# Kernel optimization log

Hardware: AMD Instinct MI355X
Metric: run time of the kernel (lower is better)

The kernel has to match this reference:

```python
import jax, jax.numpy as jnp
import numpy as np

B, N = 32, 512


def _stick_breaking(b, x_mask):
    """Row-major stick-breaking recurrence, O(N^2) sequential steps.

    Equivalent to the TF while_loop: for step in range(N*N), m=step//N, n=step%N:
      fut      = max(0, x_mask[:,m,n+1:] - sum_{m'<m} x[:,m',n+1:])  (col partial sums)
      mfm      = sum_j fut_j
      row_sum  = sum_{n'<n} x[:,m,n']
      col_sum  = sum_{m'<m} x[:,m',n]
      lower    = mask[m,n]*max(0, 1 - row_sum - mfm)
      upper    = mask[m,n]*min(1 - row_sum, 1 - col_sum)
      x[m,n]   = lower + b[m,n]*(upper - lower)
    Key insight: during row m the column partial sums are constant, so the
    future-mass terms for every n can be precomputed as an exclusive reverse
    cumsum; only the within-row dependency (row_sum) needs a scan.
    """
    Bb, Nn, _ = b.shape
    dt = b.dtype

    def row_step(col_sums, inputs):
        b_row, mask_row = inputs                      # [B, N] each
        fut = jnp.maximum(0.0, mask_row - col_sums)   # [B, N]
        # mfm[:, n] = sum_{j > n} fut[:, j]  (exclusive reverse cumsum)
        mfm = jnp.flip(jnp.cumsum(jnp.flip(fut, -1), axis=-1), -1) - fut

        def col_step(row_sum, inp):
            b_mn, m_mn, mfm_n, cs_n = inp             # [B] each
            lower = m_mn * jnp.maximum(0.0, 1.0 - row_sum - mfm_n)
            upper = m_mn * jnp.minimum(1.0 - row_sum, 1.0 - cs_n)
            p = lower + b_mn * (upper - lower)
            return row_sum + p, p

        _, row = jax.lax.scan(
            col_step,
            jnp.zeros((Bb,), dt),
            (b_row.T, mask_row.T, mfm.T, col_sums.T),
        )
        row = row.T                                   # [B, N]
        return col_sums + row, row

    _, rows = jax.lax.scan(
        row_step,
        jnp.zeros((Bb, Nn), dt),
        (jnp.swapaxes(b, 0, 1), jnp.swapaxes(x_mask, 0, 1)),
    )
    return jnp.swapaxes(rows, 0, 1)                   # [B, N, N]


def setup_inputs() -> dict:
    key = jax.random.key(0)
    k1, _ = jax.random.split(key)
    x = jax.random.normal(k1, (B, N, N), dtype=jnp.float32)
    x_mask = jnp.ones((B, N, N), dtype=jnp.float32)
    return {"x": x, "x_mask": x_mask}


def reference(x, x_mask):
    # layer.call applies sigmoid to the logits before stick-breaking
    return _stick_breaking(jax.nn.sigmoid(x), x_mask)
```

## Files before the change

kernel.cpp:

```cpp
#include <hip/hip_runtime.h>
#include <type_traits>

#define NBATCH 32
#define NDIM 512
#define NFAST 448
#define NWAVE 8


template <int CTRL, int RMASK>
__device__ __forceinline__ float dpp_add(float x) {
  int t = __builtin_amdgcn_update_dpp(0, __float_as_int(x), CTRL, RMASK, 0xf,
                                      false);
  return x + __int_as_float(t);
}

__device__ __forceinline__ float prefix_inc(float x) {
  x = dpp_add<0x111, 0xf>(x);
  x = dpp_add<0x112, 0xf>(x);
  x = dpp_add<0x114, 0xf>(x);
  x = dpp_add<0x118, 0xf>(x);
  x = dpp_add<0x142, 0xa>(x);
  x = dpp_add<0x143, 0xc>(x);
  return x;
}

__device__ __forceinline__ float wave_shr1(float x, float fill) {
  return __int_as_float(__builtin_amdgcn_update_dpp(
      __float_as_int(fill), __float_as_int(x), 0x138 , 0xf, 0xf,
      false));
}

template <int CTRL, int RMASK>
__device__ __forceinline__ void aff_step(float& A, float& B) {
  float Ae = __int_as_float(__builtin_amdgcn_update_dpp(
      __float_as_int(1.0f), __float_as_int(A), CTRL, RMASK, 0xf, false));
  float Be = __int_as_float(__builtin_amdgcn_update_dpp(
      0, __float_as_int(B), CTRL, RMASK, 0xf, false));
  B = fmaf(A, Be, B);
  A = A * Ae;
}

__device__ __forceinline__ void wg_barrier() {
  asm volatile("s_waitcnt lgkmcnt(0)" ::: "memory");
  __builtin_amdgcn_s_barrier();
  asm volatile("" ::: "memory");
}

__global__ __launch_bounds__(512, 2)
void sb_kernel(const float* __restrict__ x, const float* __restrict__ xm,
               float* __restrict__ out) {
  const int tid = (int)threadIdx.x;
  const int lane = tid & 63;
  const int w = __builtin_amdgcn_readfirstlane(tid >> 6);
  const size_t base =
      (size_t)blockIdx.x * NDIM * NDIM + (size_t)(w * 64 + lane);
  const float* xb = x + base;
  const float* mb = xm + base;
  float* ob = out + base;

  __shared__ float4 recs[NFAST];
  __shared__ alignas(16) float ex_sa[NWAVE];
  __shared__ alignas(16) float ex_S[NWAVE];
  __shared__ alignas(16) float ex_A[NWAVE];
  __shared__ alignas(16) float ex_B[NWAVE];

  float w8, t8, sa;
  float fu = 0.0f, S = 0.0f;
  float c1, c2, oc2;

  float X0 = *(xb);
  float M0 = *(mb);
  float a1 = xb[NDIM], b1 = mb[NDIM];
  float a2 = xb[2 * NDIM], b2 = mb[2 * NDIM];
  float a3 = xb[3 * NDIM], b3 = mb[3 * NDIM];
  float sx0 = a1, sm0 = b1, sx1 = a1, sm1 = b1, sx2 = a1, sm2 = b1, sx3 = a1,
        sm3 = b1;
  switch (w & 3) {
    case 0:
      sx1 = a1; sm1 = b1; sx2 = a2; sm2 = b2; sx3 = a3; sm3 = b3;
      break;
    case 1:
      sx2 = a1; sm2 = b1; sx3 = a2; sm3 = b2; sx0 = a3; sm0 = b3;
      break;
    case 2:
      sx3 = a1; sm3 = b1; sx0 = a2; sm0 = b2; sx1 = a3; sm1 = b3;
      break;
    default:
      sx0 = a1; sm0 = b1; sx1 = a2; sm1 = b2; sx2 = a3; sm2 = b3;
      break;
  }

  {
    float sg = __builtin_amdgcn_rcpf(1.0f + __expf(-X0));
    c2 = M0 * sg;
    oc2 = 1.0f - c2;
    c1 = M0 - c2;
    w8 = 1.0f;
    t8 = c2;
    sa = t8;
  }

  auto fast_step = [&](int t, float& LX, float& LM, const float& CX,
                       const float& CM) {
    const int m = t - w;
    if ((unsigned)m < (unsigned)NFAST) {
      float4 r = make_float4(1.0f, 0.0f, 0.0f, 0.0f);
      if (w > 0) r = recs[m];
      const size_t nro = (size_t)(m + 4) * NDIM;
      LX = xb[nro];
      LM = mb[nro];

      float PA = prefix_inc(sa);

      float sg = __builtin_amdgcn_rcpf(1.0f + __expf(-CX));
      float c2n = CM * sg;
      float oc2n = 1.0f - c2n;
      float c1n = CM - c2n;

      float uin = fmaxf(1.0f - (r.z + (PA - sa)), 0.0f);

      bool pW = w8 < uin;
      float A = pW ? 1.0f : oc2;
      float Bv = pW ? (-t8) : 0.0f;

      aff_step<0x111, 0xf>(A, Bv);
      aff_step<0x112, 0xf>(A, Bv);
      aff_step<0x114, 0xf>(A, Bv);
      aff_step<0x118, 0xf>(A, Bv);
      aff_step<0x142, 0xa>(A, Bv);
      aff_step<0x143, 0xc>(A, Bv);
      float Aex = wave_shr1(A, 1.0f);
      float Bex = wave_shr1(Bv, 0.0f);

      if (w < NWAVE - 1 && lane == 63)
        recs[m] = make_float4(A * r.x, fmaf(A, r.y, Bv), r.z + PA, 0.0f);

      float E = r.x + r.y;
      float e = fminf(fmaxf(fmaf(Aex, E, Bex), 0.0f), 1.0f);

      float p = c2 * fminf(e, w8);
      w8 -= p;
      ob[(size_t)m * NDIM] = p;

      t8 = c2n * w8;
      sa = t8;
      c2 = c2n;
      oc2 = oc2n;
      c1 = c1n;
    }
    wg_barrier();
  };

#pragma unroll 1
  for (int t = 0; t < NFAST + NWAVE; t += 4) {
    fast_step(t + 0, sx0, sm0, sx1, sm1);
    fast_step(t + 1, sx1, sm1, sx2, sm2);
    fast_step(t + 2, sx2, sm2, sx3, sm3);
    fast_step(t + 3, sx3, sm3, sx0, sm0);
  }

  sx1 = xb[(size_t)449 * NDIM];
  sm1 = mb[(size_t)449 * NDIM];
  sx2 = xb[(size_t)450 * NDIM];
  sm2 = mb[(size_t)450 * NDIM];
  sx3 = xb[(size_t)451 * NDIM];
  sm3 = mb[(size_t)451 * NDIM];
  {
    float om = 1.0f - c1 - c2;
    fu = fmaxf(w8 - om, 0.0f);
    S = fu;
  }

  auto row_full = [&](int m, float& WX, float& WM, const float& RX,
                      const float& RM) {
    const size_t nro = (size_t)((m + 4) & (NDIM - 1)) * NDIM;
    WX = xb[nro];
    WM = mb[nro];

    float PS = prefix_inc(S);
    float PA = prefix_inc(sa);

    if (lane == 63) {
      ex_sa[w] = PA;
      ex_S[w] = PS;
    }
    wg_barrier();

    float4 sl = *(const float4*)&ex_sa[0];
    float4 sh = *(const float4*)&ex_sa[4];
    float4 Sl = *(const float4*)&ex_S[0];
    float4 Sh = *(const float4*)&ex_S[4];
    float off_sa = 0.0f, off_S = 0.0f;
    if (w > 0) { off_sa += sl.x; off_S += Sl.x; }
    if (w > 1) { off_sa += sl.y; off_S += Sl.y; }
    if (w > 2) { off_sa += sl.z; off_S += Sl.z; }
    if (w > 3) { off_sa += sl.w; off_S += Sl.w; }
    if (w > 4) { off_sa += sh.x; off_S += Sh.x; }
    if (w > 5) { off_sa += sh.y; off_S += Sh.y; }
    if (w > 6) { off_sa += sh.z; off_S += Sh.z; }
    float Tg = ((Sl.x + Sl.y) + (Sl.z + Sl.w)) + ((Sh.x + Sh.y) + (Sh.z + Sh.w));

    float uin = fmaxf(1.0f - (off_sa + (PA - sa)), 0.0f);
    float R_ = (Tg - off_S) - PS;
    float nc1m = -c1 * R_;

    bool pW = w8 < uin;
    float aP = pW ? 1.0f : oc2;
    float bP = pW ? (-t8) : 0.0f;
    bool pL = (uin - R_) > 0.0f;
    if (pL) {
      aP -= c1;
      bP -= nc1m;
    }

    float A = aP, Bv = bP;
    aff_step<0x111, 0xf>(A, Bv);
    aff_step<0x112, 0xf>(A, Bv);
    aff_step<0x114, 0xf>(A, Bv);
    aff_step<0x118, 0xf>(A, Bv);
    aff_step<0x142, 0xa>(A, Bv);
    aff_step<0x143, 0xc>(A, Bv);
    float Aex = wave_shr1(A, 1.0f);
    float Bex = wave_shr1(Bv, 0.0f);

    if (lane == 63) {
      ex_A[w] = A;
      ex_B[w] = Bv;
    }
    wg_barrier();

    float4 Al = *(const float4*)&ex_A[0];
    float4 Ah = *(const float4*)&ex_A[4];
    float4 Bl = *(const float4*)&ex_B[0];
    float4 Bh = *(const float4*)&ex_B[4];
    float E = 1.0f;
    if (w > 0) E = fmaf(Al.x, E, Bl.x);
    if (w > 1) E = fmaf(Al.y, E, Bl.y);
    if (w > 2) E = fmaf(Al.z, E, Bl.z);
    if (w > 3) E = fmaf(Al.w, E, Bl.w);
    if (w > 4) E = fmaf(Ah.x, E, Bh.x);
    if (w > 5) E = fmaf(Ah.y, E, Bh.y);
    if (w > 6) E = fmaf(Ah.z, E, Bh.z);
    float e = fminf(fmaxf(fmaf(Aex, E, Bex), 0.0f), 1.0f);

    float sg = __builtin_amdgcn_rcpf(1.0f + __expf(-RX));
    float c2n = RM * sg;
    float oc2n = 1.0f - c2n;
    float c1n = RM - c2n;
    float omn = 1.0f - RM;

    float U = fminf(e, w8);
    float g = fmaxf(fmaf(c1, e, nc1m), 0.0f);
    float p = fmaf(c2, U, g);
    w8 -= p;
    ob[(size_t)m * NDIM] = p;

    t8 = c2n * w8;
    sa = t8;
    fu = fmaxf(w8 - omn, 0.0f);
    S = fu;
    c2 = c2n;
    oc2 = oc2n;
    c1 = c1n;
  };

#pragma unroll 1
  for (int m = NFAST; m < NDIM; m += 4) {
    row_full(m + 0, sx0, sm0, sx1, sm1);
    row_full(m + 1, sx1, sm1, sx2, sm2);
    row_full(m + 2, sx2, sm2, sx3, sm3);
    row_full(m + 3, sx3, sm3, sx0, sm0);
  }
}

extern "C" void kernel_launch(void* const* d_in, const int* in_sizes, int n_in,
                              void* d_out, int out_size, void* d_ws,
                              size_t ws_size, hipStream_t stream) {
  const float* x = (const float*)d_in[0];
  const float* xmask = (const float*)d_in[1];
  float* out = (float*)d_out;
  (void)in_sizes;
  (void)n_in;
  (void)out_size;
  (void)d_ws;
  (void)ws_size;
  hipLaunchKernelGGL(sb_kernel, dim3(NBATCH), dim3(512), 0, stream, x, xmask,
                     out);
}
```

Before: 293.8 us.

## Process two rows per wavefront pipeline step to halve workgroup barriers

The fast wavefront-skewed phase now handles a pair of consecutive rows per barrier step instead of one, so the pipeline runs 224+7 steps rather than 448+7. Loads, the sigmoid precompute and pointer arithmetic are restructured around a three-slot register rotation of row pairs, with incrementing base pointers. This is meant to cut the number of s_barrier synchronisations and the per-step overhead. The trade-off is a longer serial dependency chain within each step and a longer pipeline fill and drain per wave.

```diff
diff --git a/kernel.cpp b/kernel.cpp
--- a/kernel.cpp
+++ b/kernel.cpp
@@ -1,9 +1,9 @@
 #include <hip/hip_runtime.h>
-#include <type_traits>
 
 #define NBATCH 32
 #define NDIM 512
 #define NFAST 448
+#define NPAIR 224
 #define NWAVE 8
 
 
@@ -64,109 +64,144 @@
   __shared__ alignas(16) float ex_A[NWAVE];
   __shared__ alignas(16) float ex_B[NWAVE];
 
-  float w8, t8, sa;
+  float w8, t8;
+  float c2_0, oc2_0, c2_1, oc2_1;
+  float c1, c2, oc2;
   float fu = 0.0f, S = 0.0f;
-  float c1, c2, oc2;
-
-  float X0 = *(xb);
-  float M0 = *(mb);
-  float a1 = xb[NDIM], b1 = mb[NDIM];
-  float a2 = xb[2 * NDIM], b2 = mb[2 * NDIM];
-  float a3 = xb[3 * NDIM], b3 = mb[3 * NDIM];
-  float sx0 = a1, sm0 = b1, sx1 = a1, sm1 = b1, sx2 = a1, sm2 = b1, sx3 = a1,
-        sm3 = b1;
-  switch (w & 3) {
+
+  float X0 = xb[0], M0 = mb[0];
+  float X1 = xb[NDIM], M1 = mb[NDIM];
+  float p1x0 = xb[2 * NDIM], p1x1 = xb[3 * NDIM];
+  float p1m0 = mb[2 * NDIM], p1m1 = mb[3 * NDIM];
+  float p2x0 = xb[4 * NDIM], p2x1 = xb[5 * NDIM];
+  float p2m0 = mb[4 * NDIM], p2m1 = mb[5 * NDIM];
+
+  float Ax0, Ax1, Am0, Am1;
+  float Bx0, Bx1, Bm0, Bm1;
+  float Cx0, Cx1, Cm0, Cm1;
+  Ax0 = Bx0 = Cx0 = p1x0;
+  Ax1 = Bx1 = Cx1 = p1x1;
+  Am0 = Bm0 = Cm0 = p1m0;
+  Am1 = Bm1 = Cm1 = p1m1;
+  switch (w % 3) {
     case 0:
-      sx1 = a1; sm1 = b1; sx2 = a2; sm2 = b2; sx3 = a3; sm3 = b3;
+      Bx0 = p1x0; Bx1 = p1x1; Bm0 = p1m0; Bm1 = p1m1;
+      Cx0 = p2x0; Cx1 = p2x1; Cm0 = p2m0; Cm1 = p2m1;
       break;
     case 1:
-      sx2 = a1; sm2 = b1; sx3 = a2; sm3 = b2; sx0 = a3; sm0 = b3;
-      break;
-    case 2:
-      sx3 = a1; sm3 = b1; sx0 = a2; sm0 = b2; sx1 = a3; sm1 = b3;
+      Cx0 = p1x0; Cx1 = p1x1; Cm0 = p1m0; Cm1 = p1m1;
+      Ax0 = p2x0; Ax1 = p2x1; Am0 = p2m0; Am1 = p2m1;
       break;
     default:
-      sx0 = a1; sm0 = b1; sx1 = a2; sm1 = b2; sx2 = a3; sm2 = b3;
+      Ax0 = p1x0; Ax1 = p1x1; Am0 = p1m0; Am1 = p1m1;
+      Bx0 = p2x0; Bx1 = p2x1; Bm0 = p2m0; Bm1 = p2m1;
       break;
   }
 
   {
-    float sg = __builtin_amdgcn_rcpf(1.0f + __expf(-X0));
-    c2 = M0 * sg;
-    oc2 = 1.0f - c2;
-    c1 = M0 - c2;
+    float sg0 = __builtin_amdgcn_rcpf(1.0f + __expf(-X0));
+    c2_0 = M0 * sg0;
+    oc2_0 = 1.0f - c2_0;
+    float sg1 = __builtin_amdgcn_rcpf(1.0f + __expf(-X1));
+    c2_1 = M1 * sg1;
+    oc2_1 = 1.0f - c2_1;
     w8 = 1.0f;
-    t8 = c2;
-    sa = t8;
-  }
-
-  auto fast_step = [&](int t, float& LX, float& LM, const float& CX,
-                       const float& CM) {
-    const int m = t - w;
-    if ((unsigned)m < (unsigned)NFAST) {
-      float4 r = make_float4(1.0f, 0.0f, 0.0f, 0.0f);
-      if (w > 0) r = recs[m];
-      const size_t nro = (size_t)(m + 4) * NDIM;
-      LX = xb[nro];
-      LM = mb[nro];
-
-      float PA = prefix_inc(sa);
-
-      float sg = __builtin_amdgcn_rcpf(1.0f + __expf(-CX));
-      float c2n = CM * sg;
-      float oc2n = 1.0f - c2n;
-      float c1n = CM - c2n;
-
-      float uin = fmaxf(1.0f - (r.z + (PA - sa)), 0.0f);
-
-      bool pW = w8 < uin;
-      float A = pW ? 1.0f : oc2;
-      float Bv = pW ? (-t8) : 0.0f;
-
-      aff_step<0x111, 0xf>(A, Bv);
-      aff_step<0x112, 0xf>(A, Bv);
-      aff_step<0x114, 0xf>(A, Bv);
-      aff_step<0x118, 0xf>(A, Bv);
-      aff_step<0x142, 0xa>(A, Bv);
-      aff_step<0x143, 0xc>(A, Bv);
-      float Aex = wave_shr1(A, 1.0f);
-      float Bex = wave_shr1(Bv, 0.0f);
-
-      if (w < NWAVE - 1 && lane == 63)
-        recs[m] = make_float4(A * r.x, fmaf(A, r.y, Bv), r.z + PA, 0.0f);
-
-      float E = r.x + r.y;
-      float e = fminf(fmaxf(fmaf(Aex, E, Bex), 0.0f), 1.0f);
-
-      float p = c2 * fminf(e, w8);
-      w8 -= p;
-      ob[(size_t)m * NDIM] = p;
-
-      t8 = c2n * w8;
-      sa = t8;
-      c2 = c2n;
-      oc2 = oc2n;
-      c1 = c1n;
+    t8 = c2_0;
+  }
+
+  const float* px = xb + (long)(6 - 2 * w) * NDIM;
+  const float* pm = mb + (long)(6 - 2 * w) * NDIM;
+  float* po = ob - (long)(2 * w) * NDIM;
+
+  auto row_fast = [&](int m, const float4& r, float c2r, float oc2r,
+                      float* pO) {
+    float PA = prefix_inc(t8);
+    float uin = fmaxf(1.0f - (r.z + (PA - t8)), 0.0f);
+    bool pW = w8 < uin;
+    float A = pW ? 1.0f : oc2r;
+    float Bv = pW ? (-t8) : 0.0f;
+    aff_step<0x111, 0xf>(A, Bv);
+    aff_step<0x112, 0xf>(A, Bv);
+    aff_step<0x114, 0xf>(A, Bv);
+    aff_step<0x118, 0xf>(A, Bv);
+    aff_step<0x142, 0xa>(A, Bv);
+    aff_step<0x143, 0xc>(A, Bv);
+    float Aex = wave_shr1(A, 1.0f);
+    float Bex = wave_shr1(Bv, 0.0f);
+    if (w < NWAVE - 1 && lane == 63)
+      recs[m] = make_float4(A * r.x, fmaf(A, r.y, Bv), r.z + PA, 0.0f);
+    float E = r.x + r.y;
+    float e = fminf(fmaxf(fmaf(Aex, E, Bex), 0.0f), 1.0f);
+    float p = c2r * fminf(e, w8);
+    w8 -= p;
+    *pO = p;
+  };
+
+  auto pair_step = [&](int t, int k, float& WX0, float& WX1, float& WM0,
+                       float& WM1, const float& RX0, const float& RX1,
+                       const float& RM0, const float& RM1) {
+    const int s = t - w;
+    if ((unsigned)s < (unsigned)NPAIR) {
+      const int m = 2 * s;
+      float4 r0 = make_float4(1.0f, 0.0f, 0.0f, 0.0f), r1 = r0;
+      if (w > 0) {
+        r0 = recs[m];
+        r1 = recs[m + 1];
+      }
+      const float* pxk = px + (size_t)(2 * k) * NDIM;
+      const float* pmk = pm + (size_t)(2 * k) * NDIM;
+      float LX0 = pxk[0], LX1 = pxk[NDIM];
+      float LM0 = pmk[0], LM1 = pmk[NDIM];
+
+      float sg0 = __builtin_amdgcn_rcpf(1.0f + __expf(-RX0));
+      float c2n0 = RM0 * sg0;
+      float oc2n0 = 1.0f - c2n0;
+      float sg1 = __builtin_amdgcn_rcpf(1.0f + __expf(-RX1));
+      float c2n1 = RM1 * sg1;
+      float oc2n1 = 1.0f - c2n1;
+
+      float* pok = po + (size_t)(2 * k) * NDIM;
+      row_fast(m, r0, c2_0, oc2_0, pok);
+      t8 = c2_1 * w8;
+      row_fast(m + 1, r1, c2_1, oc2_1, pok + NDIM);
+      t8 = c2n0 * w8;
+      c2_0 = c2n0;
+      oc2_0 = oc2n0;
+      c2_1 = c2n1;
+      oc2_1 = oc2n1;
+      WX0 = LX0;
+      WX1 = LX1;
+      WM0 = LM0;
+      WM1 = LM1;
     }
     wg_barrier();
   };
 
 #pragma unroll 1
-  for (int t = 0; t < NFAST + NWAVE; t += 4) {
-    fast_step(t + 0, sx0, sm0, sx1, sm1);
-    fast_step(t + 1, sx1, sm1, sx2, sm2);
-    fast_step(t + 2, sx2, sm2, sx3, sm3);
-    fast_step(t + 3, sx3, sm3, sx0, sm0);
-  }
-
-  sx1 = xb[(size_t)449 * NDIM];
-  sm1 = mb[(size_t)449 * NDIM];
-  sx2 = xb[(size_t)450 * NDIM];
-  sm2 = mb[(size_t)450 * NDIM];
-  sx3 = xb[(size_t)451 * NDIM];
-  sm3 = mb[(size_t)451 * NDIM];
+  for (int t = 0; t < NPAIR + NWAVE - 1; t += 3) {
+    pair_step(t + 0, 0, Ax0, Ax1, Am0, Am1, Bx0, Bx1, Bm0, Bm1);
+    pair_step(t + 1, 1, Bx0, Bx1, Bm0, Bm1, Cx0, Cx1, Cm0, Cm1);
+    pair_step(t + 2, 2, Cx0, Cx1, Cm0, Cm1, Ax0, Ax1, Am0, Am1);
+    px += 6 * NDIM;
+    pm += 6 * NDIM;
+    po += 6 * NDIM;
+  }
+
+  float fx0, fm0, fx1, fm1, fx2, fm2, fx3, fm3;
   {
-    float om = 1.0f - c1 - c2;
+    float m448 = mb[(size_t)448 * NDIM];
+    fx1 = xb[(size_t)449 * NDIM];
+    fm1 = mb[(size_t)449 * NDIM];
+    fx2 = xb[(size_t)450 * NDIM];
+    fm2 = mb[(size_t)450 * NDIM];
+    fx3 = xb[(size_t)451 * NDIM];
+    fm3 = mb[(size_t)451 * NDIM];
+    fx0 = fx1;
+    fm0 = fm1;
+    c2 = c2_0;
+    oc2 = oc2_0;
+    c1 = m448 - c2;
+    float om = 1.0f - m448;
     fu = fmaxf(w8 - om, 0.0f);
     S = fu;
   }
@@ -178,7 +213,7 @@
     WM = mb[nro];
 
     float PS = prefix_inc(S);
-    float PA = prefix_inc(sa);
+    float PA = prefix_inc(t8);
 
     if (lane == 63) {
       ex_sa[w] = PA;
@@ -198,9 +233,10 @@
     if (w > 4) { off_sa += sh.x; off_S += Sh.x; }
     if (w > 5) { off_sa += sh.y; off_S += Sh.y; }
     if (w > 6) { off_sa += sh.z; off_S += Sh.z; }
-    float Tg = ((Sl.x + Sl.y) + (Sl.z + Sl.w)) + ((Sh.x + Sh.y) + (Sh.z + Sh.w));
-
-    float uin = fmaxf(1.0f - (off_sa + (PA - sa)), 0.0f);
+    float Tg =
+        ((Sl.x + Sl.y) + (Sl.z + Sl.w)) + ((Sh.x + Sh.y) + (Sh.z + Sh.w));
+
+    float uin = fmaxf(1.0f - (off_sa + (PA - t8)), 0.0f);
     float R_ = (Tg - off_S) - PS;
     float nc1m = -c1 * R_;
 
@@ -256,7 +292,6 @@
     ob[(size_t)m * NDIM] = p;
 
     t8 = c2n * w8;
-    sa = t8;
     fu = fmaxf(w8 - omn, 0.0f);
     S = fu;
     c2 = c2n;
@@ -266,10 +301,10 @@
 
 #pragma unroll 1
   for (int m = NFAST; m < NDIM; m += 4) {
-    row_full(m + 0, sx0, sm0, sx1, sm1);
-    row_full(m + 1, sx1, sm1, sx2, sm2);
-    row_full(m + 2, sx2, sm2, sx3, sm3);
-    row_full(m + 3, sx3, sm3, sx0, sm0);
+    row_full(m + 0, fx0, fm0, fx1, fm1);
+    row_full(m + 1, fx1, fm1, fx2, fm2);
+    row_full(m + 2, fx2, fm2, fx3, fm3);
+    row_full(m + 3, fx3, fm3, fx0, fm0);
   }
 }
 
```

Result: faster. 271.6 us (-7.6%).
